# Kernel tuning notes

Measured on AMD Instinct MI355X. Metric: run time of the kernel, lower is better.

Reference implementation:

```python
import jax, jax.numpy as jnp
import numpy as np

WINDOW = (6, 7, 7)  # (agent_size, window_size, window_size)
HEADS = 8           # dim // dim_head = 256 // 32


def _relative_position_index(ws):
    d, h, w = ws
    coords = np.stack(np.meshgrid(np.arange(d), np.arange(h), np.arange(w), indexing='ij'))
    cf = coords.reshape(3, -1)                      # [3, n]
    rel = cf[:, :, None] - cf[:, None, :]           # [3, n, n]
    rel = rel.transpose(1, 2, 0).copy()             # [n, n, 3]
    rel[..., 0] += d - 1
    rel[..., 1] += h - 1
    rel[..., 2] += w - 1
    rel[..., 0] *= (2 * h - 1) * (2 * w - 1)
    rel[..., 1] *= (2 * w - 1)
    return rel.sum(-1)                              # [n, n] int

REL_IDX = jnp.asarray(_relative_position_index(WINDOW))


def setup_inputs() -> dict:
    key = jax.random.key(0)
    ks = jax.random.split(key, 7)
    dim = 256
    n_bias = (2 * WINDOW[0] - 1) * (2 * WINDOW[1] - 1) * (2 * WINDOW[2] - 1)  # 1859
    s = 0.02
    return {
        'x': jax.random.normal(ks[0], (2, 6, 12, 12, 7, 7, dim), jnp.float32),
        'Wq': jax.random.normal(ks[1], (dim, dim), jnp.float32) * s,
        'bq': jax.random.normal(ks[2], (dim,), jnp.float32) * s,
        'Wkv': jax.random.normal(ks[3], (dim, 2 * dim), jnp.float32) * s,
        'bkv': jax.random.normal(ks[4], (2 * dim,), jnp.float32) * s,
        'Wout': jax.random.normal(ks[5], (dim, dim), jnp.float32) * s,
        'bias_table': jax.random.normal(ks[6], (n_bias, HEADS), jnp.float32) * s,
    }


def reference(x, Wq, bq, Wkv, bkv, Wout, bias_table):
    b, l, gx, gy, w1, w2, d = x.shape
    h = HEADS
    dh = d // h
    n = l * w1 * w2
    B = b * gx * gy
    # 'b l x y w1 w2 d -> (b x y) (l w1 w2) d'  (agent-major token order)
    xt = jnp.transpose(x, (0, 2, 3, 1, 4, 5, 6)).reshape(B, n, d)
    q = xt @ Wq + bq                                  # [B, n, d]
    kv = xt @ Wkv + bkv                               # [B, n, 2d]
    k, v = kv[..., :d], kv[..., d:]
    split = lambda t: t.reshape(B, n, h, dh).transpose(0, 2, 1, 3)  # [B, h, n, dh]
    q, k, v = split(q), split(k), split(v)
    scale = dh ** -0.5
    sim = jnp.einsum('bhid,bhjd->bhij', q * scale, k)  # [B, h, n, n]
    bias = bias_table[REL_IDX]                         # [n, n, h]
    sim = sim + jnp.transpose(bias, (2, 0, 1))[None]
    attn = jax.nn.softmax(sim, axis=-1)
    out = jnp.einsum('bhij,bhjd->bhid', attn, v)       # [B, h, n, dh]
    out = out.transpose(0, 2, 1, 3).reshape(B, n, d) @ Wout
    # '(b x y) (l w1 w2) d -> b l x y w1 w2 d'
    out = out.reshape(b, gx, gy, l, w1, w2, d)
    return jnp.transpose(out, (0, 3, 1, 2, 4, 5, 6))
```

## Files before the change

kernel.cpp:

```cpp
#include <hip/hip_runtime.h>
#include <hip/hip_bf16.h>

#define DIM    256
#define NWIN   294
#define BWIN   288
#define MROWS  (BWIN * NWIN)
#define MPAD   84736
#define NHEADS 8
#define DH     32
#define NBIAS  1859
#define QPAD   304

typedef __attribute__((ext_vector_type(8))) short  short8;
typedef __attribute__((ext_vector_type(4))) float  f32x4;

__device__ __forceinline__ unsigned short f2bf(float f) {
    unsigned int u = __float_as_uint(f);
    u += 0x7FFFu + ((u >> 16) & 1u);
    return (unsigned short)(u >> 16);
}

__device__ __forceinline__ unsigned pk2bf(float a, float b) {
    __hip_bfloat162 h = __float22bfloat162_rn(float2{a, b});
    unsigned u;
    __builtin_memcpy(&u, &h, 4);
    return u;
}

__device__ __forceinline__ void gl_lds16(const void* g, void* l) {
    __builtin_amdgcn_global_load_lds((const __attribute__((address_space(1))) unsigned int*)g,
                                     (__attribute__((address_space(3))) unsigned int*)l,
                                     16, 0, 0);
}

__global__ __launch_bounds__(256) void prep_x(const float* __restrict__ x,
                                              unsigned short* __restrict__ Xb)
{
    const int g   = blockIdx.x * 256 + threadIdx.x;
    const int row = g >> 5;
    const int col = (g & 31) * 8;
    if (row >= MPAD) return;
    uint4 pk;
    if (row < MROWS) {
        const int bw = row / NWIN, rw = row - bw * NWIN;
        const int bb = bw / 144,  r2 = bw - bb * 144;
        const int gxi = r2 / 12,  gyi = r2 - gxi * 12;
        const int lz = rw / 49,   r3 = rw - lz * 49;
        const int wa = r3 / 7,    wb = r3 - wa * 7;
        const float* src = x + ((((((size_t)bb * 6 + lz) * 12 + gxi) * 12 + gyi) * 7 + wa) * 7 + wb) * DIM + col;
        const float4 f0 = *(const float4*)(src);
        const float4 f1 = *(const float4*)(src + 4);
        pk.x = pk2bf(f0.x, f0.y);
        pk.y = pk2bf(f0.z, f0.w);
        pk.z = pk2bf(f1.x, f1.y);
        pk.w = pk2bf(f1.z, f1.w);
    } else {
        pk = (uint4){0u, 0u, 0u, 0u};
    }
    *(uint4*)(Xb + (size_t)row * 256 + col) = pk;
}

__global__ __launch_bounds__(256) void prep_w(const float* __restrict__ Wq,
                                              const float* __restrict__ Wkv,
                                              const float* __restrict__ Wout,
                                              unsigned short* __restrict__ Wt,
                                              unsigned short* __restrict__ Wot)
{
    const int g = blockIdx.x * 256 + threadIdx.x;
    if (g < 768 * 256) {
        const int n = g >> 8, k = g & 255;
        const float v = (n < 256) ? Wq[k * 256 + n] : Wkv[k * 512 + (n - 256)];
        Wt[g] = f2bf(v);
    } else {
        const int g2 = g - 768 * 256;
        const int n = g2 >> 8, k = g2 & 255;
        Wot[g2] = f2bf(Wout[k * 256 + n]);
    }
}

__global__ __launch_bounds__(256) void prep_bias(const float* __restrict__ bias_table,
                                                 float* __restrict__ biasT)
{
    const int g = blockIdx.x * 256 + threadIdx.x;
    if (g >= NHEADS * QPAD * QPAD) return;
    const int k = g % QPAD;
    const int q = (g / QPAD) % QPAD;
    const int h = g / (QPAD * QPAD);
    float v = 0.f;
    if (q < NWIN && k < NWIN) {
        const int ql = q / 49, qr = q - ql * 49, qa = qr / 7, qb = qr - qa * 7;
        const int kl = k / 49, kr = k - kl * 49, ka = kr / 7, kb = kr - ka * 7;
        const int idx = 169 * (ql - kl + 5) + 13 * (qa - ka + 6) + (qb - kb + 6);
        v = bias_table[idx * NHEADS + h] * 1.44269504088896f;
    }
    biasT[g] = v;
}

__global__ __launch_bounds__(256) void gemm_qkv(
    const unsigned short* __restrict__ Xb, const unsigned short* __restrict__ Wt,
    const float* __restrict__ bq, const float* __restrict__ bkv,
    unsigned short* __restrict__ Qb, unsigned short* __restrict__ Kb,
    unsigned short* __restrict__ Vtb)
{
    __shared__ __align__(16) unsigned short As[128 * 64];
    __shared__ __align__(16) unsigned short Bs[128 * 64];

    const int bn = blockIdx.x % 6;
    const int bm = blockIdx.x / 6;
    const int tileM = bm * 128;
    const int tileN = bn * 128;

    const int t    = threadIdx.x;
    const int w    = t >> 6;
    const int lane = t & 63;
    const int quad = lane >> 4;
    const int l15  = lane & 15;
    const int wm   = w >> 1, wn = w & 1;

    const int rA = lane >> 3;
    const int kA = (lane & 7) * 8;
    const unsigned short* aBase = Xb + ((size_t)tileM + rA) * 256 + kA;
    const unsigned short* bBase = Wt + ((size_t)tileN + rA) * 256 + kA;

    f32x4 acc[4][4] = {};

    for (int kb = 0; kb < 4; ++kb) {
        const int k0 = kb * 64;
        __syncthreads();
#pragma unroll
        for (int i = 0; i < 4; ++i) {
            const int c = w * 4 + i;
            gl_lds16(aBase + (size_t)c * 8 * 256 + k0, &As[c * 512]);
            gl_lds16(bBase + (size_t)c * 8 * 256 + k0, &Bs[c * 512]);
        }
        __syncthreads();
#pragma unroll
        for (int c2 = 0; c2 < 2; ++c2) {
            const int kk = c2 * 32 + quad * 8;
            short8 a[4], b[4];
#pragma unroll
            for (int mi = 0; mi < 4; ++mi)
                a[mi] = *(const short8*)&As[(wm * 64 + mi * 16 + l15) * 64 + kk];
#pragma unroll
            for (int ni = 0; ni < 4; ++ni)
                b[ni] = *(const short8*)&Bs[(wn * 64 + ni * 16 + l15) * 64 + kk];
#pragma unroll
            for (int mi = 0; mi < 4; ++mi)
#pragma unroll
                for (int ni = 0; ni < 4; ++ni)
                    acc[mi][ni] = __builtin_amdgcn_mfma_f32_16x16x32_bf16(a[mi], b[ni], acc[mi][ni], 0, 0, 0);
        }
    }

    const int colB = tileN + wn * 64;
    float bias[4];
#pragma unroll
    for (int ni = 0; ni < 4; ++ni) {
        const int n = colB + ni * 16 + l15;
        bias[ni] = (n < 256) ? bq[n] : bkv[n - 256];
    }
    const int rowB = tileM + wm * 64 + quad * 4;
#pragma unroll
    for (int mi = 0; mi < 4; ++mi) {
#pragma unroll
        for (int r = 0; r < 4; ++r) {
            const int row = rowB + mi * 16 + r;
            if (row < MROWS) {
                const int bw = row / NWIN;
                const int rw = row - bw * NWIN;
#pragma unroll
                for (int ni = 0; ni < 4; ++ni) {
                    const int n = colB + ni * 16 + l15;
                    const unsigned short v = f2bf(acc[mi][ni][r] + bias[ni]);
                    const int ch = n & 255;
                    const int hd = ch >> 5, di = ch & 31;
                    if (n < 512) {
                        unsigned short* dst = (n < 256) ? Qb : Kb;
                        dst[((size_t)(bw * NHEADS + hd) * NWIN + rw) * DH + di] = v;
                    } else {
                        Vtb[((size_t)(bw * NHEADS + hd) * DH + di) * NWIN + rw] = v;
                    }
                }
            }
        }
    }
}

__global__ __launch_bounds__(256, 3) void attn_kernel(
    const unsigned short* __restrict__ Qb, const unsigned short* __restrict__ Kb,
    const unsigned short* __restrict__ Vtb, const float* __restrict__ biasT,
    unsigned short* __restrict__ Ob)
{
    const int bh   = blockIdx.x;
    const int bwin = bh >> 3;
    const int h    = bh & 7;

    __shared__ __align__(16) unsigned short Ks[304 * 40];
    __shared__ __align__(16) unsigned short Vts[32 * 328];

    const int t    = threadIdx.x;
    const int w    = t >> 6;
    const int lane = t & 63;
    const int quad = lane >> 4;
    const int l15  = lane & 15;

    {
        const unsigned short* Kg = Kb + (size_t)bh * (NWIN * DH);
        for (int i = t; i < 304 * 4; i += 256) {
            const int row = i >> 2, seg = i & 3;
            uint4 v = (uint4){0u, 0u, 0u, 0u};
            if (row < NWIN) v = *(const uint4*)(Kg + row * 32 + seg * 8);
            *(uint4*)(Ks + row * 40 + seg * 8) = v;
        }
    }
    {
        const unsigned short* Vg = Vtb + (size_t)bh * (DH * NWIN);
        for (int i = t; i < 32 * 80; i += 256) {
            const int d = i / 80, c = i - d * 80;
            const int kt = c >> 3, qd = (c >> 1) & 3, hf = c & 1;
            const int kb = kt * 32 + hf * 16 + qd * 4;
            unsigned int u0 = 0u, u1 = 0u;
            if (kb + 3 < NWIN) {
                u0 = *(const unsigned int*)(Vg + d * NWIN + kb);
                u1 = *(const unsigned int*)(Vg + d * NWIN + kb + 2);
            } else if (kb < NWIN) {
                unsigned short r0 = Vg[d * NWIN + kb];
                unsigned short r1 = (kb + 1 < NWIN) ? Vg[d * NWIN + kb + 1] : (unsigned short)0;
                unsigned short r2 = (kb + 2 < NWIN) ? Vg[d * NWIN + kb + 2] : (unsigned short)0;
                u0 = (unsigned int)r0 | ((unsigned int)r1 << 16);
                u1 = (unsigned int)r2;
            }
            unsigned int* dst = (unsigned int*)(Vts + d * 328 + c * 4);
            dst[0] = u0; dst[1] = u1;
        }
    }
    __syncthreads();

    const float SL2E = 0.25503486f;
    const unsigned short* Qg = Qb + (size_t)bh * (NWIN * DH);
    const float* biasH = biasT + (size_t)h * QPAD * QPAD;
    const short8 ones = (short8){0x3F80,0x3F80,0x3F80,0x3F80,0x3F80,0x3F80,0x3F80,0x3F80};

#pragma unroll
    for (int r5 = 0; r5 < 5; ++r5) {
        const int it = 4 * r5 + w;
        if (it < 19) {
            short8 qf;
            const int qrow = it * 16 + l15;
            if (qrow < NWIN) qf = *(const short8*)(Qg + qrow * DH + quad * 8);
            else             qf = (short8){0,0,0,0,0,0,0,0};

            const float* bb = biasH + (size_t)qrow * QPAD;

            f32x4 S[19];
#pragma unroll
            for (int jt = 0; jt < 19; ++jt) {
                const short8 kf = *(const short8*)(Ks + (jt * 16 + l15) * 40 + quad * 8);
                S[jt] = __builtin_amdgcn_mfma_f32_16x16x32_bf16(kf, qf, (f32x4){0.f,0.f,0.f,0.f}, 0, 0, 0);
            }

            unsigned pk0[20], pk1[20];
            pk0[19] = 0u; pk1[19] = 0u;
#pragma unroll
            for (int jt = 0; jt < 19; ++jt) {
                const f32x4 b4 = *(const f32x4*)(bb + jt * 16 + quad * 4);
                float p0 = exp2f(fmaf(S[jt][0], SL2E, b4[0]));
                float p1 = exp2f(fmaf(S[jt][1], SL2E, b4[1]));
                float p2 = exp2f(fmaf(S[jt][2], SL2E, b4[2]));
                float p3 = exp2f(fmaf(S[jt][3], SL2E, b4[3]));
                if (jt == 18) {
                    if (quad * 4 + 0 >= 6) p0 = 0.f;
                    if (quad * 4 + 1 >= 6) p1 = 0.f;
                    if (quad * 4 + 2 >= 6) p2 = 0.f;
                    if (quad * 4 + 3 >= 6) p3 = 0.f;
                }
                pk0[jt] = pk2bf(p0, p1);
                pk1[jt] = pk2bf(p2, p3);
            }

            f32x4 o0 = {0.f,0.f,0.f,0.f}, o1 = {0.f,0.f,0.f,0.f}, o2 = {0.f,0.f,0.f,0.f};
#pragma unroll
            for (int kt = 0; kt < 10; ++kt) {
                uint4 pw;
                pw.x = pk0[2 * kt];
                pw.y = pk1[2 * kt];
                pw.z = pk0[2 * kt + 1];
                pw.w = pk1[2 * kt + 1];
                short8 pa;
                __builtin_memcpy(&pa, &pw, 16);
                const short8 v0 = *(const short8*)(Vts + l15 * 328 + kt * 32 + quad * 8);
                const short8 v1 = *(const short8*)(Vts + (16 + l15) * 328 + kt * 32 + quad * 8);
                o0 = __builtin_amdgcn_mfma_f32_16x16x32_bf16(pa, v0, o0, 0, 0, 0);
                o1 = __builtin_amdgcn_mfma_f32_16x16x32_bf16(pa, v1, o1, 0, 0, 0);
                o2 = __builtin_amdgcn_mfma_f32_16x16x32_bf16(pa, ones, o2, 0, 0, 0);
            }

#pragma unroll
            for (int r = 0; r < 4; ++r) {
                const int rg = it * 16 + quad * 4 + r;
                if (rg < NWIN) {
                    const float inv = 1.0f / o2[r];
                    unsigned short* op = Ob + ((size_t)bwin * NWIN + rg) * DIM + h * DH;
                    op[l15]      = f2bf(o0[r] * inv);
                    op[16 + l15] = f2bf(o1[r] * inv);
                }
            }
        }
    }
}

__global__ __launch_bounds__(256) void gemm_out(
    const unsigned short* __restrict__ Ob, const unsigned short* __restrict__ Wot,
    float* __restrict__ out)
{
    __shared__ __align__(16) unsigned short As[128 * 64];
    __shared__ __align__(16) unsigned short Bs[128 * 64];

    const int bn = blockIdx.x & 1;
    const int bm = blockIdx.x >> 1;
    const int tileM = bm * 128;
    const int tileN = bn * 128;

    const int t    = threadIdx.x;
    const int w    = t >> 6;
    const int lane = t & 63;
    const int quad = lane >> 4;
    const int l15  = lane & 15;
    const int wm   = w >> 1, wn = w & 1;

    const int rA = lane >> 3;
    const int kA = (lane & 7) * 8;
    const unsigned short* aBase = Ob  + ((size_t)tileM + rA) * 256 + kA;
    const unsigned short* bBase = Wot + ((size_t)tileN + rA) * 256 + kA;

    f32x4 acc[4][4] = {};

    for (int kb = 0; kb < 4; ++kb) {
        const int k0 = kb * 64;
        __syncthreads();
#pragma unroll
        for (int i = 0; i < 4; ++i) {
            const int c = w * 4 + i;
            gl_lds16(aBase + (size_t)c * 8 * 256 + k0, &As[c * 512]);
            gl_lds16(bBase + (size_t)c * 8 * 256 + k0, &Bs[c * 512]);
        }
        __syncthreads();
#pragma unroll
        for (int c2 = 0; c2 < 2; ++c2) {
            const int kk = c2 * 32 + quad * 8;
            short8 a[4], b[4];
#pragma unroll
            for (int mi = 0; mi < 4; ++mi)
                a[mi] = *(const short8*)&As[(wm * 64 + mi * 16 + l15) * 64 + kk];
#pragma unroll
            for (int ni = 0; ni < 4; ++ni)
                b[ni] = *(const short8*)&Bs[(wn * 64 + ni * 16 + l15) * 64 + kk];
#pragma unroll
            for (int mi = 0; mi < 4; ++mi)
#pragma unroll
                for (int ni = 0; ni < 4; ++ni)
                    acc[mi][ni] = __builtin_amdgcn_mfma_f32_16x16x32_bf16(a[mi], b[ni], acc[mi][ni], 0, 0, 0);
        }
    }

    const int colB = tileN + wn * 64;
    const int rowB = tileM + wm * 64 + quad * 4;
#pragma unroll
    for (int mi = 0; mi < 4; ++mi) {
#pragma unroll
        for (int r = 0; r < 4; ++r) {
            const int row = rowB + mi * 16 + r;
            if (row < MROWS) {
                const int bw = row / NWIN, rw = row - bw * NWIN;
                const int bb = bw / 144,  r2 = bw - bb * 144;
                const int gxi = r2 / 12,  gyi = r2 - gxi * 12;
                const int lz = rw / 49,   r3 = rw - lz * 49;
                const int wa = r3 / 7,    wb = r3 - wa * 7;
                float* orow = out + ((((((size_t)bb * 6 + lz) * 12 + gxi) * 12 + gyi) * 7 + wa) * 7 + wb) * DIM;
#pragma unroll
                for (int ni = 0; ni < 4; ++ni)
                    orow[colB + ni * 16 + l15] = acc[mi][ni][r];
            }
        }
    }
}

extern "C" void kernel_launch(void* const* d_in, const int* in_sizes, int n_in,
                              void* d_out, int out_size, void* d_ws, size_t ws_size,
                              hipStream_t stream)
{
    const float* x          = (const float*)d_in[0];
    const float* Wq         = (const float*)d_in[1];
    const float* bq         = (const float*)d_in[2];
    const float* Wkv        = (const float*)d_in[3];
    const float* bkv        = (const float*)d_in[4];
    const float* Wout       = (const float*)d_in[5];
    const float* bias_table = (const float*)d_in[6];
    float* out = (float*)d_out;

    const size_t planePad = (size_t)MPAD * DIM;
    const size_t plane    = (size_t)MROWS * DIM;
    unsigned short* Xb  = (unsigned short*)d_ws;
    unsigned short* Qb  = Xb + planePad;
    unsigned short* Kb  = Qb + plane;
    unsigned short* Vtb = Kb + plane;
    unsigned short* Ob  = Vtb + plane;
    unsigned short* Wt  = Ob + planePad;
    unsigned short* Wot = Wt + 768 * 256;
    float*          biasT = (float*)(Wot + 256 * 256);

    prep_x<<<MPAD / 8, 256, 0, stream>>>(x, Xb);
    prep_w<<<1024, 256, 0, stream>>>(Wq, Wkv, Wout, Wt, Wot);
    prep_bias<<<(NHEADS * QPAD * QPAD + 255) / 256, 256, 0, stream>>>(bias_table, biasT);
    gemm_qkv<<<662 * 6, 256, 0, stream>>>(Xb, Wt, bq, bkv, Qb, Kb, Vtb);
    attn_kernel<<<BWIN * NHEADS, 256, 0, stream>>>(Qb, Kb, Vtb, biasT, Ob);
    gemm_out<<<662 * 2, 256, 0, stream>>>(Ob, Wot, out);
}
```

Baseline: 406.0 us.

## Double-buffer GEMM LDS tiles, swizzle workgroups across XCDs, vectorize QKV epilogue stores

Both projection GEMMs now stage K-tiles into two LDS buffers, prefetching the next tile while MFMAs run on the current one. Workgroup IDs are remapped so consecutive tiles land on the same XCD, which should improve L2 reuse of the shared A rows. The QKV epilogue computes the window and row index once per 4-row group and writes V transposed as packed bf16 pairs, with a slow path for groups that cross a window boundary. LDS use per block doubles, which may lower occupancy.

```diff
diff --git a/kernel.cpp b/kernel.cpp
--- a/kernel.cpp
+++ b/kernel.cpp
@@ -31,6 +31,44 @@
     __builtin_amdgcn_global_load_lds((const __attribute__((address_space(1))) unsigned int*)g,
                                      (__attribute__((address_space(3))) unsigned int*)l,
                                      16, 0, 0);
+}
+
+__device__ __forceinline__ int xcd_swizzle(int orig, int nwg) {
+    const int xcd = orig & 7, idx = orig >> 3;
+    const int q = nwg >> 3, r = nwg & 7;
+    return (xcd < r) ? (xcd * (q + 1) + idx) : (r * (q + 1) + (xcd - r) * q + idx);
+}
+
+__device__ __forceinline__ void stage_tile(const unsigned short* aBase, const unsigned short* bBase,
+                                           unsigned short* As_, unsigned short* Bs_, int w, int k0)
+{
+#pragma unroll
+    for (int i = 0; i < 4; ++i) {
+        const int c = w * 4 + i;
+        gl_lds16(aBase + (size_t)c * 8 * 256 + k0, As_ + c * 512);
+        gl_lds16(bBase + (size_t)c * 8 * 256 + k0, Bs_ + c * 512);
+    }
+}
+
+__device__ __forceinline__ void tile_mfma(const unsigned short* As_, const unsigned short* Bs_,
+                                          int wm, int wn, int quad, int l15, f32x4 (&acc)[4][4])
+{
+#pragma unroll
+    for (int c2 = 0; c2 < 2; ++c2) {
+        const int kk = c2 * 32 + quad * 8;
+        short8 a[4], b[4];
+#pragma unroll
+        for (int mi = 0; mi < 4; ++mi)
+            a[mi] = *(const short8*)&As_[(wm * 64 + mi * 16 + l15) * 64 + kk];
+#pragma unroll
+        for (int ni = 0; ni < 4; ++ni)
+            b[ni] = *(const short8*)&Bs_[(wn * 64 + ni * 16 + l15) * 64 + kk];
+#pragma unroll
+        for (int mi = 0; mi < 4; ++mi)
+#pragma unroll
+            for (int ni = 0; ni < 4; ++ni)
+                acc[mi][ni] = __builtin_amdgcn_mfma_f32_16x16x32_bf16(a[mi], b[ni], acc[mi][ni], 0, 0, 0);
+    }
 }
 
 __global__ __launch_bounds__(256) void prep_x(const float* __restrict__ x,
@@ -102,11 +140,12 @@
     unsigned short* __restrict__ Qb, unsigned short* __restrict__ Kb,
     unsigned short* __restrict__ Vtb)
 {
-    __shared__ __align__(16) unsigned short As[128 * 64];
-    __shared__ __align__(16) unsigned short Bs[128 * 64];
-
-    const int bn = blockIdx.x % 6;
-    const int bm = blockIdx.x / 6;
+    __shared__ __align__(16) unsigned short As[2][128 * 64];
+    __shared__ __align__(16) unsigned short Bs[2][128 * 64];
+
+    const int wg = xcd_swizzle(blockIdx.x, 662 * 6);
+    const int bn = wg % 6;
+    const int bm = wg / 6;
     const int tileM = bm * 128;
     const int tileN = bn * 128;
 
@@ -124,33 +163,16 @@
 
     f32x4 acc[4][4] = {};
 
-    for (int kb = 0; kb < 4; ++kb) {
-        const int k0 = kb * 64;
+    stage_tile(aBase, bBase, As[0], Bs[0], w, 0);
+    __syncthreads();
+#pragma unroll
+    for (int kb = 0; kb < 3; ++kb) {
+        const int cur = kb & 1;
+        stage_tile(aBase, bBase, As[cur ^ 1], Bs[cur ^ 1], w, (kb + 1) * 64);
+        tile_mfma(As[cur], Bs[cur], wm, wn, quad, l15, acc);
         __syncthreads();
-#pragma unroll
-        for (int i = 0; i < 4; ++i) {
-            const int c = w * 4 + i;
-            gl_lds16(aBase + (size_t)c * 8 * 256 + k0, &As[c * 512]);
-            gl_lds16(bBase + (size_t)c * 8 * 256 + k0, &Bs[c * 512]);
-        }
-        __syncthreads();
-#pragma unroll
-        for (int c2 = 0; c2 < 2; ++c2) {
-            const int kk = c2 * 32 + quad * 8;
-            short8 a[4], b[4];
-#pragma unroll
-            for (int mi = 0; mi < 4; ++mi)
-                a[mi] = *(const short8*)&As[(wm * 64 + mi * 16 + l15) * 64 + kk];
-#pragma unroll
-            for (int ni = 0; ni < 4; ++ni)
-                b[ni] = *(const short8*)&Bs[(wn * 64 + ni * 16 + l15) * 64 + kk];
-#pragma unroll
-            for (int mi = 0; mi < 4; ++mi)
-#pragma unroll
-                for (int ni = 0; ni < 4; ++ni)
-                    acc[mi][ni] = __builtin_amdgcn_mfma_f32_16x16x32_bf16(a[mi], b[ni], acc[mi][ni], 0, 0, 0);
-        }
-    }
+    }
+    tile_mfma(As[1], Bs[1], wm, wn, quad, l15, acc);
 
     const int colB = tileN + wn * 64;
     float bias[4];
@@ -162,23 +184,51 @@
     const int rowB = tileM + wm * 64 + quad * 4;
 #pragma unroll
     for (int mi = 0; mi < 4; ++mi) {
-#pragma unroll
-        for (int r = 0; r < 4; ++r) {
-            const int row = rowB + mi * 16 + r;
-            if (row < MROWS) {
-                const int bw = row / NWIN;
-                const int rw = row - bw * NWIN;
-#pragma unroll
-                for (int ni = 0; ni < 4; ++ni) {
-                    const int n = colB + ni * 16 + l15;
-                    const unsigned short v = f2bf(acc[mi][ni][r] + bias[ni]);
-                    const int ch = n & 255;
-                    const int hd = ch >> 5, di = ch & 31;
-                    if (n < 512) {
-                        unsigned short* dst = (n < 256) ? Qb : Kb;
-                        dst[((size_t)(bw * NHEADS + hd) * NWIN + rw) * DH + di] = v;
+        const int row0 = rowB + mi * 16;
+        if (row0 < MROWS) {
+            const int bw0 = row0 / NWIN;
+            const int rw0 = row0 - bw0 * NWIN;
+            const bool same = (rw0 <= NWIN - 4);
+#pragma unroll
+            for (int ni = 0; ni < 4; ++ni) {
+                const int n = colB + ni * 16 + l15;
+                const int ch = n & 255;
+                const int hd = ch >> 5, di = ch & 31;
+                if (n < 512) {
+                    unsigned short* dst = (n < 256) ? Qb : Kb;
+                    if (same) {
+                        unsigned short* p = dst + ((size_t)(bw0 * NHEADS + hd) * NWIN + rw0) * DH + di;
+#pragma unroll
+                        for (int r = 0; r < 4; ++r)
+                            p[r * DH] = f2bf(acc[mi][ni][r] + bias[ni]);
                     } else {
-                        Vtb[((size_t)(bw * NHEADS + hd) * DH + di) * NWIN + rw] = v;
+#pragma unroll
+                        for (int r = 0; r < 4; ++r) {
+                            const int row = row0 + r;
+                            if (row < MROWS) {
+                                const int bw = row / NWIN, rw = row - bw * NWIN;
+                                dst[((size_t)(bw * NHEADS + hd) * NWIN + rw) * DH + di] =
+                                    f2bf(acc[mi][ni][r] + bias[ni]);
+                            }
+                        }
+                    }
+                } else {
+                    if (same) {
+                        unsigned short* p = Vtb + ((size_t)(bw0 * NHEADS + hd) * DH + di) * NWIN + rw0;
+                        const unsigned lo = pk2bf(acc[mi][ni][0] + bias[ni], acc[mi][ni][1] + bias[ni]);
+                        const unsigned hi = pk2bf(acc[mi][ni][2] + bias[ni], acc[mi][ni][3] + bias[ni]);
+                        *(unsigned*)(p)     = lo;
+                        *(unsigned*)(p + 2) = hi;
+                    } else {
+#pragma unroll
+                        for (int r = 0; r < 4; ++r) {
+                            const int row = row0 + r;
+                            if (row < MROWS) {
+                                const int bw = row / NWIN, rw = row - bw * NWIN;
+                                Vtb[((size_t)(bw * NHEADS + hd) * DH + di) * NWIN + rw] =
+                                    f2bf(acc[mi][ni][r] + bias[ni]);
+                            }
+                        }
                     }
                 }
             }
@@ -313,11 +363,12 @@
     const unsigned short* __restrict__ Ob, const unsigned short* __restrict__ Wot,
     float* __restrict__ out)
 {
-    __shared__ __align__(16) unsigned short As[128 * 64];
-    __shared__ __align__(16) unsigned short Bs[128 * 64];
-
-    const int bn = blockIdx.x & 1;
-    const int bm = blockIdx.x >> 1;
+    __shared__ __align__(16) unsigned short As[2][128 * 64];
+    __shared__ __align__(16) unsigned short Bs[2][128 * 64];
+
+    const int wg = xcd_swizzle(blockIdx.x, 662 * 2);
+    const int bn = wg & 1;
+    const int bm = wg >> 1;
     const int tileM = bm * 128;
     const int tileN = bn * 128;
 
@@ -335,33 +386,16 @@
 
     f32x4 acc[4][4] = {};
 
-    for (int kb = 0; kb < 4; ++kb) {
-        const int k0 = kb * 64;
+    stage_tile(aBase, bBase, As[0], Bs[0], w, 0);
+    __syncthreads();
+#pragma unroll
+    for (int kb = 0; kb < 3; ++kb) {
+        const int cur = kb & 1;
+        stage_tile(aBase, bBase, As[cur ^ 1], Bs[cur ^ 1], w, (kb + 1) * 64);
+        tile_mfma(As[cur], Bs[cur], wm, wn, quad, l15, acc);
         __syncthreads();
-#pragma unroll
-        for (int i = 0; i < 4; ++i) {
-            const int c = w * 4 + i;
-            gl_lds16(aBase + (size_t)c * 8 * 256 + k0, &As[c * 512]);
-            gl_lds16(bBase + (size_t)c * 8 * 256 + k0, &Bs[c * 512]);
-        }
-        __syncthreads();
-#pragma unroll
-        for (int c2 = 0; c2 < 2; ++c2) {
-            const int kk = c2 * 32 + quad * 8;
-            short8 a[4], b[4];
-#pragma unroll
-            for (int mi = 0; mi < 4; ++mi)
-                a[mi] = *(const short8*)&As[(wm * 64 + mi * 16 + l15) * 64 + kk];
-#pragma unroll
-            for (int ni = 0; ni < 4; ++ni)
-                b[ni] = *(const short8*)&Bs[(wn * 64 + ni * 16 + l15) * 64 + kk];
-#pragma unroll
-            for (int mi = 0; mi < 4; ++mi)
-#pragma unroll
-                for (int ni = 0; ni < 4; ++ni)
-                    acc[mi][ni] = __builtin_amdgcn_mfma_f32_16x16x32_bf16(a[mi], b[ni], acc[mi][ni], 0, 0, 0);
-        }
-    }
+    }
+    tile_mfma(As[1], Bs[1], wm, wn, quad, l15, acc);
 
     const int colB = tileN + wn * 64;
     const int rowB = tileM + wm * 64 + quad * 4;
```

Measured after the change: 375.2 us. 7.6% less time.
